# Optimization experiments

Hardware: AMD Instinct MI355X
Metric: run time of the kernel (lower is better)

## Reference

```python
import jax, jax.numpy as jnp
import numpy as np

B, N, IN_DIM, L_DIM, H_DIM, N_CLASSES, FLOW_LEN = 128, 512, 128, 64, 64, 10, 4


def setup_inputs() -> dict:
    key = jax.random.key(0)
    ks = jax.random.split(key, 20)
    s = 0.05
    return {
        "gs": jax.random.uniform(ks[0], (B, N, N), dtype=jnp.float32),
        "hs": jax.random.normal(ks[1], (B, N, IN_DIM), dtype=jnp.float32),
        "labels": jax.random.randint(ks[2], (B,), 0, N_CLASSES),
        "eps": jax.random.normal(ks[3], (B, N, 1), dtype=jnp.float32),
        "W_s": jax.random.normal(ks[4], (IN_DIM, L_DIM), dtype=jnp.float32) * s,
        "b_s": jnp.zeros((L_DIM,), jnp.float32),
        "W_mu": jax.random.normal(ks[5], (L_DIM, 1), dtype=jnp.float32) * s,
        "b_mu": jnp.zeros((1,), jnp.float32),
        "W_lv": jax.random.normal(ks[6], (L_DIM, 1), dtype=jnp.float32) * s,
        "b_lv": jnp.zeros((1,), jnp.float32),
        "W_dec": jax.random.normal(ks[7], (1, L_DIM), dtype=jnp.float32) * s,
        "b_dec": jnp.zeros((L_DIM,), jnp.float32),
        "W1": jax.random.normal(ks[8], (L_DIM, H_DIM), dtype=jnp.float32) * s,
        "b1": jnp.zeros((H_DIM,), jnp.float32),
        "W2": jax.random.normal(ks[9], (H_DIM, N_CLASSES), dtype=jnp.float32) * s,
        "b2": jnp.zeros((N_CLASSES,), jnp.float32),
        "beta": jax.random.uniform(ks[10], (1,), jnp.float32, 0.0, 100.0),
        "fw": jax.random.normal(ks[11], (FLOW_LEN,), dtype=jnp.float32) * 0.1,
        "fb": jax.random.normal(ks[12], (FLOW_LEN,), dtype=jnp.float32) * 0.1,
        "fs": jax.random.normal(ks[13], (FLOW_LEN,), dtype=jnp.float32) * 0.1,
    }


def reference(gs, hs, labels, eps, W_s, b_s, W_mu, b_mu, W_lv, b_lv,
              W_dec, b_dec, W1, b1, W2, b2, beta, fw, fb, fs):
    relu = jax.nn.relu
    # norm_g: g / g.sum(1) (torch broadcast divides column j by row-sum deg[j])
    deg = gs.sum(axis=2)                       # [B, N]
    g = gs / deg[:, None, :]                   # [B, N, N]

    def gcn(g, h, W, b):
        return relu(jnp.einsum('bij,bjf->bif', g, h) @ W + b)

    h = gcn(g, hs, W_s, b_s)                   # [B, N, L]
    r = h
    mu = gcn(g, h, W_mu, b_mu)                 # [B, N, 1]
    logvar = gcn(g, h, W_lv, b_lv)             # [B, N, 1]
    sigma = jnp.exp(0.5 * logvar)
    z0 = eps * sigma + mu                      # reparameterize (training)

    # 4-step planar flow on scalar latent; log-det accumulated on pre-transform z
    z = z0
    log_jac = jnp.zeros_like(z0)
    for k in range(FLOW_LEN):
        t = jnp.tanh(fw[k] * z + fb[k])
        det = 1.0 + fs[k] * fw[k] * (1.0 - t * t)
        log_jac = log_jac + jnp.log(jnp.abs(det) + 1e-7)
        z = z + fs[k] * t
    zk = z

    # KL = log q(z0) - log_jac - log p(zk), loggaussian = -0.5*((z-mu)/s)^2 - log(2.5 s)
    logq = -0.5 * ((z0 - mu) / sigma) ** 2 - jnp.log(2.5 * sigma)
    logp = -0.5 * zk ** 2 - jnp.log(jnp.float32(2.5))
    kl = logq - log_jac - logp                 # [B, N, 1]

    zs = jax.nn.sigmoid(beta * zk)             # [B, N, 1]
    d = gcn(g, zs, W_dec, b_dec)               # [B, N, L]
    hg = jnp.einsum('bnl,bn->bl', h, zs[..., 0])  # h.T @ zk, [B, L]

    # classify
    x = relu(hg @ W1 + b1)
    logits = jax.nn.log_softmax(x @ W2 + b2, axis=1)  # [B, C]

    nll = -jnp.mean(logits[jnp.arange(B), labels])
    mse = jnp.mean((r - d) ** 2)
    loss = nll + mse + kl.mean()
    preds = jnp.argmax(logits, axis=1)
    acc = jnp.mean((preds == labels).astype(jnp.float32))
    return jnp.stack([loss, acc])
```

## Files before the change

### kernel.cpp

```cpp
#include <hip/hip_runtime.h>
#include <hip/hip_bf16.h>

#define BB 128
#define NN 512
#define IND 128
#define LD 64
#define NC 10
#define FL 4
#define ROWS (BB*NN)

#define OFF_ACC 0
#define OFF_GSB 8
#define WS_NEED ((size_t)(OFF_GSB + (size_t)ROWS*256) * 4)

typedef __attribute__((ext_vector_type(8))) short short8v;
typedef __attribute__((ext_vector_type(4))) float f32x4;

__device__ inline float wave_reduce(float v) {
    #pragma unroll
    for (int m = 32; m; m >>= 1) v += __shfl_xor(v, m, 64);
    return v;
}

__device__ inline short f2bf(float f) {
    unsigned u = __float_as_uint(f);
    u += 0x7fff + ((u >> 16) & 1);
    return (short)(u >> 16);
}

__device__ inline float bf2f(short s) {
    return __uint_as_float(((unsigned)(unsigned short)s) << 16);
}

__global__ void k_zero(float* __restrict__ accums) {
    if (threadIdx.x < 8) accums[threadIdx.x] = 0.f;
}

template<bool BF>
__global__ __launch_bounds__(1024) void k_fused(
    const float* __restrict__ gs, const float* __restrict__ hs,
    const int* __restrict__ labels, const float* __restrict__ eps,
    const float* __restrict__ W_s, const float* __restrict__ b_s,
    const float* __restrict__ W_mu, const float* __restrict__ b_mu,
    const float* __restrict__ W_lv, const float* __restrict__ b_lv,
    const float* __restrict__ W_dec, const float* __restrict__ b_dec,
    const float* __restrict__ W1, const float* __restrict__ b1,
    const float* __restrict__ W2, const float* __restrict__ b2,
    const float* __restrict__ beta, const float* __restrict__ fw,
    const float* __restrict__ fb, const float* __restrict__ fs,
    unsigned short* __restrict__ gsb,
    float* __restrict__ accums, float* __restrict__ out)
{
    __shared__ unsigned short s_hwT[64 * 512];
    __shared__ unsigned short s_h[512 * 64];
    __shared__ float s_rdeg[NN];
    __shared__ float s_vm[NN], s_vv[NN];
    __shared__ float s_zs[NN], s_zss[NN];
    __shared__ float s_red[16 * 68];
    __shared__ float s_fin[48];

    const int tid = threadIdx.x, lane = tid & 63, wid = tid >> 6;
    const int b = blockIdx.x;

    for (int r = 0; r < 32; ++r) {
        int row = wid * 32 + r;
        const float4* gp = (const float4*)(gs + ((size_t)b * NN + row) * NN) + lane * 2;
        float4 a = gp[0], c = gp[1];
        float ssum = a.x + a.y + a.z + a.w + c.x + c.y + c.z + c.w;
        ssum = wave_reduce(ssum);
        if (lane == 0) s_rdeg[row] = 1.f / ssum;
        if constexpr (BF) {
            short8v v;
            v[0] = f2bf(a.x); v[1] = f2bf(a.y); v[2] = f2bf(a.z); v[3] = f2bf(a.w);
            v[4] = f2bf(c.x); v[5] = f2bf(c.y); v[6] = f2bf(c.z); v[7] = f2bf(c.w);
            *(short8v*)(gsb + ((size_t)b * NN + row) * NN + lane * 8) = v;
        }
    }

    unsigned short* sWT = s_h;
    {
        const float4* wp = (const float4*)W_s + tid * 2;
        float4 w0 = wp[0], w1 = wp[1];
        int k = tid >> 3, l0 = (tid & 7) * 8;
        float wv[8] = {w0.x, w0.y, w0.z, w0.w, w1.x, w1.y, w1.z, w1.w};
        #pragma unroll
        for (int e = 0; e < 8; ++e) {
            int l = l0 + e;
            int byte = (l * 256 + k * 2) ^ ((l & 7) << 4);
            *(unsigned short*)((char*)sWT + byte) = (unsigned short)f2bf(wv[e]);
        }
    }
    __syncthreads();

    {
        int n0 = wid * 32, cq = lane & 15, koq = lane >> 4;
        f32x4 accB[2][4] = {};
        #pragma unroll
        for (int kk = 0; kk < 4; ++kk) {
            short8v bf[4];
            #pragma unroll
            for (int lt = 0; lt < 4; ++lt) {
                int l = lt * 16 + cq;
                int byte = (l * 256 + (kk * 32 + koq * 8) * 2) ^ ((l & 7) << 4);
                bf[lt] = *(const short8v*)((char*)sWT + byte);
            }
            #pragma unroll
            for (int nt = 0; nt < 2; ++nt) {
                int row = n0 + nt * 16 + cq;
                const float4* hp = (const float4*)(hs + ((size_t)b * NN + row) * IND
                                                   + kk * 32 + koq * 8);
                float4 h0 = hp[0], h1 = hp[1];
                short8v a;
                a[0] = f2bf(h0.x); a[1] = f2bf(h0.y); a[2] = f2bf(h0.z); a[3] = f2bf(h0.w);
                a[4] = f2bf(h1.x); a[5] = f2bf(h1.y); a[6] = f2bf(h1.z); a[7] = f2bf(h1.w);
                #pragma unroll
                for (int lt = 0; lt < 4; ++lt)
                    accB[nt][lt] = __builtin_amdgcn_mfma_f32_16x16x32_bf16(a, bf[lt], accB[nt][lt], 0, 0, 0);
            }
        }
        int r0 = (lane >> 4) * 4;
        #pragma unroll
        for (int nt = 0; nt < 2; ++nt)
            #pragma unroll
            for (int lt = 0; lt < 4; ++lt)
                #pragma unroll
                for (int q = 0; q < 4; ++q) {
                    int n = n0 + nt * 16 + r0 + q;
                    int l = lt * 16 + cq;
                    int byte = (l * 1024 + n * 2) ^ ((l & 7) << 4);
                    *(unsigned short*)((char*)s_hwT + byte) =
                        (unsigned short)f2bf(accB[nt][lt][q] * s_rdeg[n]);
                }
    }
    __syncthreads();

    {
        int n0 = wid * 32, cq = lane & 15, koq = lane >> 4;
        f32x4 accC[2][4] = {};
        for (int kk = 0; kk < 16; ++kk) {
            short8v bf[4];
            #pragma unroll
            for (int lt = 0; lt < 4; ++lt) {
                int l = lt * 16 + cq;
                int byte = (l * 1024 + (kk * 32 + koq * 8) * 2) ^ ((l & 7) << 4);
                bf[lt] = *(const short8v*)((char*)s_hwT + byte);
            }
            #pragma unroll
            for (int nt = 0; nt < 2; ++nt) {
                int row = n0 + nt * 16 + cq;
                short8v a;
                if constexpr (BF) {
                    a = *(const short8v*)(gsb + ((size_t)b * NN + row) * NN + kk * 32 + koq * 8);
                } else {
                    const float4* gp = (const float4*)(gs + ((size_t)b * NN + row) * NN
                                                       + kk * 32 + koq * 8);
                    float4 g0 = gp[0], g1 = gp[1];
                    a[0] = f2bf(g0.x); a[1] = f2bf(g0.y); a[2] = f2bf(g0.z); a[3] = f2bf(g0.w);
                    a[4] = f2bf(g1.x); a[5] = f2bf(g1.y); a[6] = f2bf(g1.z); a[7] = f2bf(g1.w);
                }
                #pragma unroll
                for (int lt = 0; lt < 4; ++lt)
                    accC[nt][lt] = __builtin_amdgcn_mfma_f32_16x16x32_bf16(a, bf[lt], accC[nt][lt], 0, 0, 0);
            }
        }
        int r0 = (lane >> 4) * 4;
        float bsv[4];
        #pragma unroll
        for (int lt = 0; lt < 4; ++lt) bsv[lt] = b_s[lt * 16 + cq];
        #pragma unroll
        for (int nt = 0; nt < 2; ++nt)
            #pragma unroll
            for (int lt = 0; lt < 4; ++lt)
                #pragma unroll
                for (int q = 0; q < 4; ++q) {
                    int n = n0 + nt * 16 + r0 + q;
                    int l = lt * 16 + cq;
                    s_h[n * 64 + l] = (unsigned short)f2bf(fmaxf(accC[nt][lt][q] + bsv[lt], 0.f));
                }
    }
    __syncthreads();

    {
        int g16 = tid >> 4, l16 = tid & 15;
        float wmu[4], wlv[4];
        #pragma unroll
        for (int e = 0; e < 4; ++e) { wmu[e] = W_mu[l16 * 4 + e]; wlv[e] = W_lv[l16 * 4 + e]; }
        #pragma unroll
        for (int rr = 0; rr < 8; ++rr) {
            int row = g16 * 8 + rr;
            const unsigned short* hp = &s_h[row * 64 + l16 * 4];
            float pm = 0.f, pv = 0.f;
            #pragma unroll
            for (int e = 0; e < 4; ++e) {
                float hv = bf2f((short)hp[e]);
                pm += hv * wmu[e]; pv += hv * wlv[e];
            }
            #pragma unroll
            for (int m = 1; m <= 8; m <<= 1) {
                pm += __shfl_xor(pm, m, 64);
                pv += __shfl_xor(pv, m, 64);
            }
            if (l16 == 0) {
                float rd = s_rdeg[row];
                s_vm[row] = pm * rd;
                s_vv[row] = pv * rd;
            }
        }
    }
    __syncthreads();

    {
        float vmr[8], vvr[8];
        #pragma unroll
        for (int e = 0; e < 8; ++e) { vmr[e] = s_vm[lane * 8 + e]; vvr[e] = s_vv[lane * 8 + e]; }
        for (int r = 0; r < 32; ++r) {
            int row = wid * 32 + r;
            float sm, sv;
            if constexpr (BF) {
                short8v g8 = *(const short8v*)(gsb + ((size_t)b * NN + row) * NN + lane * 8);
                float g0 = bf2f(g8[0]), g1 = bf2f(g8[1]), g2 = bf2f(g8[2]), g3 = bf2f(g8[3]);
                float g4 = bf2f(g8[4]), g5 = bf2f(g8[5]), g6 = bf2f(g8[6]), g7 = bf2f(g8[7]);
                sm = g0*vmr[0]+g1*vmr[1]+g2*vmr[2]+g3*vmr[3]+g4*vmr[4]+g5*vmr[5]+g6*vmr[6]+g7*vmr[7];
                sv = g0*vvr[0]+g1*vvr[1]+g2*vvr[2]+g3*vvr[3]+g4*vvr[4]+g5*vvr[5]+g6*vvr[6]+g7*vvr[7];
            } else {
                const float4* gp = (const float4*)(gs + ((size_t)b * NN + row) * NN) + lane * 2;
                float4 ga = gp[0], gc = gp[1];
                sm = ga.x*vmr[0]+ga.y*vmr[1]+ga.z*vmr[2]+ga.w*vmr[3]
                   + gc.x*vmr[4]+gc.y*vmr[5]+gc.z*vmr[6]+gc.w*vmr[7];
                sv = ga.x*vvr[0]+ga.y*vvr[1]+ga.z*vvr[2]+ga.w*vvr[3]
                   + gc.x*vvr[4]+gc.y*vvr[5]+gc.z*vvr[6]+gc.w*vvr[7];
            }
            sm = wave_reduce(sm);
            sv = wave_reduce(sv);
            if (lane == 0) { s_zs[row] = sm; s_zss[row] = sv; }
        }
    }
    __syncthreads();

    float my_kl = 0.f;
    if (tid < NN) {
        float sm = s_zs[tid], sv = s_zss[tid];
        float mu = fmaxf(sm + b_mu[0], 0.f);
        float lv = fmaxf(sv + b_lv[0], 0.f);
        float sigma = expf(0.5f * lv);
        float z0 = eps[(size_t)b * NN + tid] * sigma + mu;
        float z = z0, lj = 0.f;
        #pragma unroll
        for (int k = 0; k < FL; ++k) {
            float tt = tanhf(fw[k] * z + fb[k]);
            float det = 1.f + fs[k] * fw[k] * (1.f - tt * tt);
            lj += logf(fabsf(det) + 1e-7f);
            z += fs[k] * tt;
        }
        float e0 = (z0 - mu) / sigma;
        float logq = -0.5f * e0 * e0 - logf(2.5f * sigma);
        float logp = -0.5f * z * z - logf(2.5f);
        my_kl = logq - lj - logp;
        float zv = 1.f / (1.f + expf(-beta[0] * z));
        s_zs[tid] = zv;
        s_zss[tid] = zv * s_rdeg[tid];
    }
    __syncthreads();

    float msacc = 0.f;
    {
        float wd = W_dec[lane], bd = b_dec[lane];
        float zr[8];
        #pragma unroll
        for (int e = 0; e < 8; ++e) zr[e] = s_zss[lane * 8 + e];
        for (int r = 0; r < 32; ++r) {
            int row = wid * 32 + r;
            float s;
            if constexpr (BF) {
                short8v g8 = *(const short8v*)(gsb + ((size_t)b * NN + row) * NN + lane * 8);
                s = bf2f(g8[0])*zr[0]+bf2f(g8[1])*zr[1]+bf2f(g8[2])*zr[2]+bf2f(g8[3])*zr[3]
                  + bf2f(g8[4])*zr[4]+bf2f(g8[5])*zr[5]+bf2f(g8[6])*zr[6]+bf2f(g8[7])*zr[7];
            } else {
                const float4* gp = (const float4*)(gs + ((size_t)b * NN + row) * NN) + lane * 2;
                float4 ga = gp[0], gc = gp[1];
                s = ga.x*zr[0]+ga.y*zr[1]+ga.z*zr[2]+ga.w*zr[3]
                  + gc.x*zr[4]+gc.y*zr[5]+gc.z*zr[6]+gc.w*zr[7];
            }
            s = wave_reduce(s);
            float dval = fmaxf(s * wd + bd, 0.f);
            float diff = bf2f((short)s_h[row * 64 + lane]) - dval;
            msacc += diff * diff;
        }
    }

    {
        float acc = 0.f;
        for (int r = 0; r < 32; ++r) {
            int row = wid * 32 + r;
            acc += bf2f((short)s_h[row * 64 + lane]) * s_zs[row];
        }
        s_red[wid * 68 + lane] = acc;
    }
    __syncthreads();

    {
        float kv = wave_reduce(my_kl);
        float mv = wave_reduce(msacc);
        if (lane == 0) { s_fin[wid] = kv; s_fin[16 + wid] = mv; }
    }
    if (wid == 0) {
        float hgv = 0.f;
        #pragma unroll
        for (int w = 0; w < 16; ++w) hgv += s_red[w * 68 + lane];
        s_red[lane] = hgv;
        float x = b1[lane];
        #pragma unroll 8
        for (int k = 0; k < LD; ++k) x += s_red[k] * W1[k * LD + lane];
        x = fmaxf(x, 0.f);
        s_red[256 + lane] = x;
        if (lane < NC) {
            float lg = b2[lane];
            #pragma unroll 8
            for (int k = 0; k < LD; ++k) lg += s_red[256 + k] * W2[k * NC + lane];
            s_fin[32 + lane] = lg;
        }
        if (lane == 0) {
            float mx = s_fin[32]; int pred = 0;
            #pragma unroll
            for (int c = 1; c < NC; ++c) if (s_fin[32 + c] > mx) { mx = s_fin[32 + c]; pred = c; }
            float se = 0.f;
            #pragma unroll
            for (int c = 0; c < NC; ++c) se += expf(s_fin[32 + c] - mx);
            int lab = labels[b];
            s_fin[44] = -(s_fin[32 + lab] - (mx + logf(se)));
            s_fin[45] = (pred == lab) ? 1.f : 0.f;
        }
    }
    __syncthreads();

    if (tid == 0) {
        float ksum = 0.f, msum = 0.f;
        #pragma unroll
        for (int w = 0; w < 16; ++w) { ksum += s_fin[w]; msum += s_fin[16 + w]; }
        atomicAdd(&accums[0], ksum);
        atomicAdd(&accums[1], msum);
        atomicAdd(&accums[2], s_fin[44]);
        atomicAdd(&accums[3], s_fin[45]);
        __threadfence();
        unsigned old = atomicAdd((unsigned*)&accums[4], 1u);
        if (old == BB - 1) {
            float kk = atomicAdd(&accums[0], 0.f);
            float mm = atomicAdd(&accums[1], 0.f);
            float nn = atomicAdd(&accums[2], 0.f);
            float aa = atomicAdd(&accums[3], 0.f);
            out[0] = nn / (float)BB
                   + mm / ((float)BB * NN * LD)
                   + kk / ((float)BB * NN);
            out[1] = aa / (float)BB;
        }
    }
}

extern "C" void kernel_launch(void* const* d_in, const int* in_sizes, int n_in,
                              void* d_out, int out_size, void* d_ws, size_t ws_size,
                              hipStream_t stream) {
    const float* gs    = (const float*)d_in[0];
    const float* hs    = (const float*)d_in[1];
    const int*   labels= (const int*)d_in[2];
    const float* eps   = (const float*)d_in[3];
    const float* W_s   = (const float*)d_in[4];
    const float* b_s   = (const float*)d_in[5];
    const float* W_mu  = (const float*)d_in[6];
    const float* b_mu  = (const float*)d_in[7];
    const float* W_lv  = (const float*)d_in[8];
    const float* b_lv  = (const float*)d_in[9];
    const float* W_dec = (const float*)d_in[10];
    const float* b_dec = (const float*)d_in[11];
    const float* W1    = (const float*)d_in[12];
    const float* b1    = (const float*)d_in[13];
    const float* W2    = (const float*)d_in[14];
    const float* b2    = (const float*)d_in[15];
    const float* beta  = (const float*)d_in[16];
    const float* fw    = (const float*)d_in[17];
    const float* fb    = (const float*)d_in[18];
    const float* fs    = (const float*)d_in[19];

    float* ws = (float*)d_ws;
    float* accums = ws + OFF_ACC;
    unsigned short* gsb = (unsigned short*)(ws + OFF_GSB);
    float* out = (float*)d_out;

    k_zero<<<1, 64, 0, stream>>>(accums);
    if (ws_size >= WS_NEED) {
        k_fused<true><<<BB, 1024, 0, stream>>>(gs, hs, labels, eps, W_s, b_s, W_mu, b_mu,
                                               W_lv, b_lv, W_dec, b_dec, W1, b1, W2, b2,
                                               beta, fw, fb, fs, gsb, accums, out);
    } else {
        k_fused<false><<<BB, 1024, 0, stream>>>(gs, hs, labels, eps, W_s, b_s, W_mu, b_mu,
                                                W_lv, b_lv, W_dec, b_dec, W1, b1, W2, b2,
                                                beta, fw, fb, fs, gsb, accums, out);
    }
}
```

Measured before the change: 116.8 us.

## Split fused per-batch kernel into multi-stage kernels with two blocks per graph

Replaces the single fused kernel (one 1024-thread block per graph) with a chain of kernels. A wide degree/bf16-conversion kernel is followed by GEMM, mu/flow, decoder and classifier kernels, each launching two blocks per graph that split the 512 rows. The aim is to fill more compute units than the 128 blocks did and to parallelise the degree pass across the whole device. In exchange, intermediates (h, vm/vv, zs, rdeg, partial hg) go through global workspace, there are extra launches, and each half-block recomputes the full h·W product.

```diff
diff --git a/kernel.cpp b/kernel.cpp
--- a/kernel.cpp
+++ b/kernel.cpp
@@ -8,9 +8,17 @@
 #define NC 10
 #define FL 4
 #define ROWS (BB*NN)
+#define HALF 256
 
 #define OFF_ACC 0
-#define OFF_GSB 8
+#define OFF_RDEG (OFF_ACC + 8)
+#define OFF_VM   (OFF_RDEG + ROWS)
+#define OFF_VV   (OFF_VM + ROWS)
+#define OFF_ZS   (OFF_VV + ROWS)
+#define OFF_ZSS  (OFF_ZS + ROWS)
+#define OFF_XHG  (OFF_ZSS + ROWS)
+#define OFF_H    (OFF_XHG + BB*128)
+#define OFF_GSB  (OFF_H + ROWS*32)
 #define WS_NEED ((size_t)(OFF_GSB + (size_t)ROWS*256) * 4)
 
 typedef __attribute__((ext_vector_type(8))) short short8v;
@@ -32,50 +40,43 @@
     return __uint_as_float(((unsigned)(unsigned short)s) << 16);
 }
 
-__global__ void k_zero(float* __restrict__ accums) {
-    if (threadIdx.x < 8) accums[threadIdx.x] = 0.f;
+__global__ __launch_bounds__(256) void k_deg(const float* __restrict__ gs,
+                                             float* __restrict__ rdeg,
+                                             float* __restrict__ accums,
+                                             unsigned short* __restrict__ gsb) {
+    if (blockIdx.x == 0 && threadIdx.x < 8) accums[threadIdx.x] = 0.f;
+    int t = threadIdx.x;
+    int row = blockIdx.x * 4 + (t >> 6), lane = t & 63;
+    const float4* r4 = (const float4*)(gs + (size_t)row * NN) + lane * 2;
+    float4 a = r4[0], b = r4[1];
+    float s = a.x + a.y + a.z + a.w + b.x + b.y + b.z + b.w;
+    float sr = wave_reduce(s);
+    if (lane == 0) rdeg[row] = 1.0f / sr;
+    if (gsb) {
+        short8v v;
+        v[0] = f2bf(a.x); v[1] = f2bf(a.y); v[2] = f2bf(a.z); v[3] = f2bf(a.w);
+        v[4] = f2bf(b.x); v[5] = f2bf(b.y); v[6] = f2bf(b.z); v[7] = f2bf(b.w);
+        *(short8v*)(gsb + (size_t)row * NN + lane * 8) = v;
+    }
 }
 
 template<bool BF>
-__global__ __launch_bounds__(1024) void k_fused(
-    const float* __restrict__ gs, const float* __restrict__ hs,
-    const int* __restrict__ labels, const float* __restrict__ eps,
-    const float* __restrict__ W_s, const float* __restrict__ b_s,
-    const float* __restrict__ W_mu, const float* __restrict__ b_mu,
-    const float* __restrict__ W_lv, const float* __restrict__ b_lv,
-    const float* __restrict__ W_dec, const float* __restrict__ b_dec,
-    const float* __restrict__ W1, const float* __restrict__ b1,
-    const float* __restrict__ W2, const float* __restrict__ b2,
-    const float* __restrict__ beta, const float* __restrict__ fw,
-    const float* __restrict__ fb, const float* __restrict__ fs,
-    unsigned short* __restrict__ gsb,
-    float* __restrict__ accums, float* __restrict__ out)
+__global__ __launch_bounds__(1024) void k_hwgemm(
+    const float* __restrict__ gs, const unsigned short* __restrict__ gsb,
+    const float* __restrict__ hs, const float* __restrict__ W_s,
+    const float* __restrict__ b_s, const float* __restrict__ W_mu,
+    const float* __restrict__ W_lv, const float* __restrict__ rdeg_ws,
+    unsigned short* __restrict__ h_ws, float* __restrict__ vm_ws,
+    float* __restrict__ vv_ws)
 {
     __shared__ unsigned short s_hwT[64 * 512];
-    __shared__ unsigned short s_h[512 * 64];
+    __shared__ unsigned short s_h[HALF * 64];
     __shared__ float s_rdeg[NN];
-    __shared__ float s_vm[NN], s_vv[NN];
-    __shared__ float s_zs[NN], s_zss[NN];
-    __shared__ float s_red[16 * 68];
-    __shared__ float s_fin[48];
 
     const int tid = threadIdx.x, lane = tid & 63, wid = tid >> 6;
-    const int b = blockIdx.x;
-
-    for (int r = 0; r < 32; ++r) {
-        int row = wid * 32 + r;
-        const float4* gp = (const float4*)(gs + ((size_t)b * NN + row) * NN) + lane * 2;
-        float4 a = gp[0], c = gp[1];
-        float ssum = a.x + a.y + a.z + a.w + c.x + c.y + c.z + c.w;
-        ssum = wave_reduce(ssum);
-        if (lane == 0) s_rdeg[row] = 1.f / ssum;
-        if constexpr (BF) {
-            short8v v;
-            v[0] = f2bf(a.x); v[1] = f2bf(a.y); v[2] = f2bf(a.z); v[3] = f2bf(a.w);
-            v[4] = f2bf(c.x); v[5] = f2bf(c.y); v[6] = f2bf(c.z); v[7] = f2bf(c.w);
-            *(short8v*)(gsb + ((size_t)b * NN + row) * NN + lane * 8) = v;
-        }
-    }
+    const int b = blockIdx.x >> 1, p = blockIdx.x & 1, rbase = p * HALF;
+
+    if (tid < NN) s_rdeg[tid] = rdeg_ws[(size_t)b * NN + tid];
 
     unsigned short* sWT = s_h;
     {
@@ -118,6 +119,7 @@
                     accB[nt][lt] = __builtin_amdgcn_mfma_f32_16x16x32_bf16(a, bf[lt], accB[nt][lt], 0, 0, 0);
             }
         }
+        __syncthreads();
         int r0 = (lane >> 4) * 4;
         #pragma unroll
         for (int nt = 0; nt < 2; ++nt)
@@ -135,8 +137,11 @@
     __syncthreads();
 
     {
-        int n0 = wid * 32, cq = lane & 15, koq = lane >> 4;
-        f32x4 accC[2][4] = {};
+        int cq = lane & 15, koq = lane >> 4;
+        int rowl = wid * 16 + cq, rowg = rbase + rowl;
+        const unsigned short* A16 = gsb + ((size_t)b * NN + rowg) * NN + koq * 8;
+        const float* A32 = gs + ((size_t)b * NN + rowg) * NN + koq * 8;
+        f32x4 accC[4] = {};
         for (int kk = 0; kk < 16; ++kk) {
             short8v bf[4];
             #pragma unroll
@@ -145,40 +150,41 @@
                 int byte = (l * 1024 + (kk * 32 + koq * 8) * 2) ^ ((l & 7) << 4);
                 bf[lt] = *(const short8v*)((char*)s_hwT + byte);
             }
-            #pragma unroll
-            for (int nt = 0; nt < 2; ++nt) {
-                int row = n0 + nt * 16 + cq;
-                short8v a;
-                if constexpr (BF) {
-                    a = *(const short8v*)(gsb + ((size_t)b * NN + row) * NN + kk * 32 + koq * 8);
-                } else {
-                    const float4* gp = (const float4*)(gs + ((size_t)b * NN + row) * NN
-                                                       + kk * 32 + koq * 8);
-                    float4 g0 = gp[0], g1 = gp[1];
-                    a[0] = f2bf(g0.x); a[1] = f2bf(g0.y); a[2] = f2bf(g0.z); a[3] = f2bf(g0.w);
-                    a[4] = f2bf(g1.x); a[5] = f2bf(g1.y); a[6] = f2bf(g1.z); a[7] = f2bf(g1.w);
-                }
-                #pragma unroll
-                for (int lt = 0; lt < 4; ++lt)
-                    accC[nt][lt] = __builtin_amdgcn_mfma_f32_16x16x32_bf16(a, bf[lt], accC[nt][lt], 0, 0, 0);
-            }
+            short8v a;
+            if constexpr (BF) {
+                a = *(const short8v*)(A16 + kk * 32);
+            } else {
+                const float4* gp = (const float4*)(A32 + kk * 32);
+                float4 g0 = gp[0], g1 = gp[1];
+                a[0] = f2bf(g0.x); a[1] = f2bf(g0.y); a[2] = f2bf(g0.z); a[3] = f2bf(g0.w);
+                a[4] = f2bf(g1.x); a[5] = f2bf(g1.y); a[6] = f2bf(g1.z); a[7] = f2bf(g1.w);
+            }
+            #pragma unroll
+            for (int lt = 0; lt < 4; ++lt)
+                accC[lt] = __builtin_amdgcn_mfma_f32_16x16x32_bf16(a, bf[lt], accC[lt], 0, 0, 0);
         }
         int r0 = (lane >> 4) * 4;
         float bsv[4];
         #pragma unroll
         for (int lt = 0; lt < 4; ++lt) bsv[lt] = b_s[lt * 16 + cq];
         #pragma unroll
-        for (int nt = 0; nt < 2; ++nt)
-            #pragma unroll
-            for (int lt = 0; lt < 4; ++lt)
-                #pragma unroll
-                for (int q = 0; q < 4; ++q) {
-                    int n = n0 + nt * 16 + r0 + q;
-                    int l = lt * 16 + cq;
-                    s_h[n * 64 + l] = (unsigned short)f2bf(fmaxf(accC[nt][lt][q] + bsv[lt], 0.f));
-                }
-    }
-    __syncthreads();
+        for (int lt = 0; lt < 4; ++lt)
+            #pragma unroll
+            for (int q = 0; q < 4; ++q) {
+                int nloc = wid * 16 + r0 + q;
+                int l = lt * 16 + cq;
+                s_h[nloc * 64 + l] = (unsigned short)f2bf(fmaxf(accC[lt][q] + bsv[lt], 0.f));
+            }
+    }
+    __syncthreads();
+
+    {
+        int rowl = tid >> 2, off = (tid & 3) * 16;
+        unsigned short* dst = h_ws + ((size_t)(b * NN + rbase + rowl)) * 64 + off;
+        const unsigned short* src = &s_h[rowl * 64 + off];
+        *(short8v*)dst = *(const short8v*)src;
+        *(short8v*)(dst + 8) = *(const short8v*)(src + 8);
+    }
 
     {
         int g16 = tid >> 4, l16 = tid & 15;
@@ -186,9 +192,9 @@
         #pragma unroll
         for (int e = 0; e < 4; ++e) { wmu[e] = W_mu[l16 * 4 + e]; wlv[e] = W_lv[l16 * 4 + e]; }
         #pragma unroll
-        for (int rr = 0; rr < 8; ++rr) {
-            int row = g16 * 8 + rr;
-            const unsigned short* hp = &s_h[row * 64 + l16 * 4];
+        for (int rr = 0; rr < 4; ++rr) {
+            int rowl = g16 * 4 + rr;
+            const unsigned short* hp = &s_h[rowl * 64 + l16 * 4];
             float pm = 0.f, pv = 0.f;
             #pragma unroll
             for (int e = 0; e < 4; ++e) {
@@ -201,49 +207,66 @@
                 pv += __shfl_xor(pv, m, 64);
             }
             if (l16 == 0) {
-                float rd = s_rdeg[row];
-                s_vm[row] = pm * rd;
-                s_vv[row] = pv * rd;
-            }
-        }
-    }
-    __syncthreads();
-
-    {
-        float vmr[8], vvr[8];
-        #pragma unroll
-        for (int e = 0; e < 8; ++e) { vmr[e] = s_vm[lane * 8 + e]; vvr[e] = s_vv[lane * 8 + e]; }
-        for (int r = 0; r < 32; ++r) {
-            int row = wid * 32 + r;
-            float sm, sv;
-            if constexpr (BF) {
-                short8v g8 = *(const short8v*)(gsb + ((size_t)b * NN + row) * NN + lane * 8);
-                float g0 = bf2f(g8[0]), g1 = bf2f(g8[1]), g2 = bf2f(g8[2]), g3 = bf2f(g8[3]);
-                float g4 = bf2f(g8[4]), g5 = bf2f(g8[5]), g6 = bf2f(g8[6]), g7 = bf2f(g8[7]);
-                sm = g0*vmr[0]+g1*vmr[1]+g2*vmr[2]+g3*vmr[3]+g4*vmr[4]+g5*vmr[5]+g6*vmr[6]+g7*vmr[7];
-                sv = g0*vvr[0]+g1*vvr[1]+g2*vvr[2]+g3*vvr[3]+g4*vvr[4]+g5*vvr[5]+g6*vvr[6]+g7*vvr[7];
-            } else {
-                const float4* gp = (const float4*)(gs + ((size_t)b * NN + row) * NN) + lane * 2;
-                float4 ga = gp[0], gc = gp[1];
-                sm = ga.x*vmr[0]+ga.y*vmr[1]+ga.z*vmr[2]+ga.w*vmr[3]
-                   + gc.x*vmr[4]+gc.y*vmr[5]+gc.z*vmr[6]+gc.w*vmr[7];
-                sv = ga.x*vvr[0]+ga.y*vvr[1]+ga.z*vvr[2]+ga.w*vvr[3]
-                   + gc.x*vvr[4]+gc.y*vvr[5]+gc.z*vvr[6]+gc.w*vvr[7];
-            }
-            sm = wave_reduce(sm);
-            sv = wave_reduce(sv);
-            if (lane == 0) { s_zs[row] = sm; s_zss[row] = sv; }
-        }
+                float rd = s_rdeg[rbase + rowl];
+                vm_ws[(size_t)b * NN + rbase + rowl] = pm * rd;
+                vv_ws[(size_t)b * NN + rbase + rowl] = pv * rd;
+            }
+        }
+    }
+}
+
+template<bool BF>
+__global__ __launch_bounds__(1024) void k_muflow(
+    const float* __restrict__ gs, const unsigned short* __restrict__ gsb,
+    const float* __restrict__ vm_ws, const float* __restrict__ vv_ws,
+    const float* __restrict__ eps, const float* __restrict__ b_mu,
+    const float* __restrict__ b_lv, const float* __restrict__ beta,
+    const float* __restrict__ fw, const float* __restrict__ fb,
+    const float* __restrict__ fs, const float* __restrict__ rdeg_ws,
+    float* __restrict__ zs_ws, float* __restrict__ zss_ws,
+    float* __restrict__ accums)
+{
+    __shared__ float s_mp[HALF], s_lp[HALF];
+    __shared__ float s_fin[16];
+    const int tid = threadIdx.x, lane = tid & 63, wid = tid >> 6;
+    const int b = blockIdx.x >> 1, p = blockIdx.x & 1, rbase = p * HALF;
+
+    float vmr[8], vvr[8];
+    #pragma unroll
+    for (int e = 0; e < 8; ++e) {
+        vmr[e] = vm_ws[(size_t)b * NN + lane * 8 + e];
+        vvr[e] = vv_ws[(size_t)b * NN + lane * 8 + e];
+    }
+    for (int r = 0; r < 16; ++r) {
+        int rowl = wid * 16 + r, rowg = rbase + rowl;
+        float sm, sv;
+        if constexpr (BF) {
+            short8v g8 = *(const short8v*)(gsb + ((size_t)b * NN + rowg) * NN + lane * 8);
+            float g0 = bf2f(g8[0]), g1 = bf2f(g8[1]), g2 = bf2f(g8[2]), g3 = bf2f(g8[3]);
+            float g4 = bf2f(g8[4]), g5 = bf2f(g8[5]), g6 = bf2f(g8[6]), g7 = bf2f(g8[7]);
+            sm = g0*vmr[0]+g1*vmr[1]+g2*vmr[2]+g3*vmr[3]+g4*vmr[4]+g5*vmr[5]+g6*vmr[6]+g7*vmr[7];
+            sv = g0*vvr[0]+g1*vvr[1]+g2*vvr[2]+g3*vvr[3]+g4*vvr[4]+g5*vvr[5]+g6*vvr[6]+g7*vvr[7];
+        } else {
+            const float4* gp = (const float4*)(gs + ((size_t)b * NN + rowg) * NN) + lane * 2;
+            float4 ga = gp[0], gc = gp[1];
+            sm = ga.x*vmr[0]+ga.y*vmr[1]+ga.z*vmr[2]+ga.w*vmr[3]
+               + gc.x*vmr[4]+gc.y*vmr[5]+gc.z*vmr[6]+gc.w*vmr[7];
+            sv = ga.x*vvr[0]+ga.y*vvr[1]+ga.z*vvr[2]+ga.w*vvr[3]
+               + gc.x*vvr[4]+gc.y*vvr[5]+gc.z*vvr[6]+gc.w*vvr[7];
+        }
+        sm = wave_reduce(sm);
+        sv = wave_reduce(sv);
+        if (lane == 0) { s_mp[rowl] = sm; s_lp[rowl] = sv; }
     }
     __syncthreads();
 
     float my_kl = 0.f;
-    if (tid < NN) {
-        float sm = s_zs[tid], sv = s_zss[tid];
-        float mu = fmaxf(sm + b_mu[0], 0.f);
-        float lv = fmaxf(sv + b_lv[0], 0.f);
+    if (tid < HALF) {
+        int rowg = rbase + tid;
+        float mu = fmaxf(s_mp[tid] + b_mu[0], 0.f);
+        float lv = fmaxf(s_lp[tid] + b_lv[0], 0.f);
         float sigma = expf(0.5f * lv);
-        float z0 = eps[(size_t)b * NN + tid] * sigma + mu;
+        float z0 = eps[(size_t)b * NN + rowg] * sigma + mu;
         float z = z0, lj = 0.f;
         #pragma unroll
         for (int k = 0; k < FL; ++k) {
@@ -257,90 +280,116 @@
         float logp = -0.5f * z * z - logf(2.5f);
         my_kl = logq - lj - logp;
         float zv = 1.f / (1.f + expf(-beta[0] * z));
-        s_zs[tid] = zv;
-        s_zss[tid] = zv * s_rdeg[tid];
-    }
-    __syncthreads();
-
-    float msacc = 0.f;
-    {
-        float wd = W_dec[lane], bd = b_dec[lane];
-        float zr[8];
-        #pragma unroll
-        for (int e = 0; e < 8; ++e) zr[e] = s_zss[lane * 8 + e];
-        for (int r = 0; r < 32; ++r) {
-            int row = wid * 32 + r;
-            float s;
-            if constexpr (BF) {
-                short8v g8 = *(const short8v*)(gsb + ((size_t)b * NN + row) * NN + lane * 8);
-                s = bf2f(g8[0])*zr[0]+bf2f(g8[1])*zr[1]+bf2f(g8[2])*zr[2]+bf2f(g8[3])*zr[3]
-                  + bf2f(g8[4])*zr[4]+bf2f(g8[5])*zr[5]+bf2f(g8[6])*zr[6]+bf2f(g8[7])*zr[7];
-            } else {
-                const float4* gp = (const float4*)(gs + ((size_t)b * NN + row) * NN) + lane * 2;
-                float4 ga = gp[0], gc = gp[1];
-                s = ga.x*zr[0]+ga.y*zr[1]+ga.z*zr[2]+ga.w*zr[3]
-                  + gc.x*zr[4]+gc.y*zr[5]+gc.z*zr[6]+gc.w*zr[7];
-            }
-            s = wave_reduce(s);
-            float dval = fmaxf(s * wd + bd, 0.f);
-            float diff = bf2f((short)s_h[row * 64 + lane]) - dval;
-            msacc += diff * diff;
-        }
-    }
-
-    {
-        float acc = 0.f;
-        for (int r = 0; r < 32; ++r) {
-            int row = wid * 32 + r;
-            acc += bf2f((short)s_h[row * 64 + lane]) * s_zs[row];
-        }
-        s_red[wid * 68 + lane] = acc;
-    }
-    __syncthreads();
-
-    {
-        float kv = wave_reduce(my_kl);
-        float mv = wave_reduce(msacc);
-        if (lane == 0) { s_fin[wid] = kv; s_fin[16 + wid] = mv; }
+        float rd = rdeg_ws[(size_t)b * NN + rowg];
+        zs_ws[(size_t)b * NN + rowg] = zv;
+        zss_ws[(size_t)b * NN + rowg] = zv * rd;
+    }
+    float kv = wave_reduce(my_kl);
+    if (lane == 0) s_fin[wid] = kv;
+    __syncthreads();
+    if (tid == 0) {
+        float ks = 0.f;
+        #pragma unroll
+        for (int w = 0; w < 16; ++w) ks += s_fin[w];
+        atomicAdd(&accums[0], ks);
+    }
+}
+
+template<bool BF>
+__global__ __launch_bounds__(1024) void k_dec(
+    const float* __restrict__ gs, const unsigned short* __restrict__ gsb,
+    const float* __restrict__ zss_ws, const float* __restrict__ zs_ws,
+    const unsigned short* __restrict__ h_ws, const float* __restrict__ W_dec,
+    const float* __restrict__ b_dec, float* __restrict__ accums,
+    float* __restrict__ xhg)
+{
+    __shared__ float s_zs[HALF];
+    __shared__ float s_red[16 * 68];
+    __shared__ float s_fin[16];
+    const int tid = threadIdx.x, lane = tid & 63, wid = tid >> 6;
+    const int b = blockIdx.x >> 1, p = blockIdx.x & 1, rbase = p * HALF;
+
+    if (tid < HALF) s_zs[tid] = zs_ws[(size_t)b * NN + rbase + tid];
+    float zr[8];
+    #pragma unroll
+    for (int e = 0; e < 8; ++e) zr[e] = zss_ws[(size_t)b * NN + lane * 8 + e];
+    float wd = W_dec[lane], bd = b_dec[lane];
+    __syncthreads();
+
+    float msacc = 0.f, hgacc = 0.f;
+    for (int r = 0; r < 16; ++r) {
+        int rowl = wid * 16 + r, rowg = rbase + rowl;
+        float s;
+        if constexpr (BF) {
+            short8v g8 = *(const short8v*)(gsb + ((size_t)b * NN + rowg) * NN + lane * 8);
+            s = bf2f(g8[0])*zr[0]+bf2f(g8[1])*zr[1]+bf2f(g8[2])*zr[2]+bf2f(g8[3])*zr[3]
+              + bf2f(g8[4])*zr[4]+bf2f(g8[5])*zr[5]+bf2f(g8[6])*zr[6]+bf2f(g8[7])*zr[7];
+        } else {
+            const float4* gp = (const float4*)(gs + ((size_t)b * NN + rowg) * NN) + lane * 2;
+            float4 ga = gp[0], gc = gp[1];
+            s = ga.x*zr[0]+ga.y*zr[1]+ga.z*zr[2]+ga.w*zr[3]
+              + gc.x*zr[4]+gc.y*zr[5]+gc.z*zr[6]+gc.w*zr[7];
+        }
+        s = wave_reduce(s);
+        float dval = fmaxf(s * wd + bd, 0.f);
+        float hval = bf2f((short)h_ws[((size_t)b * NN + rowg) * 64 + lane]);
+        float diff = hval - dval;
+        msacc += diff * diff;
+        hgacc += hval * s_zs[rowl];
+    }
+    s_red[wid * 68 + lane] = hgacc;
+    float mv = wave_reduce(msacc);
+    if (lane == 0) s_fin[wid] = mv;
+    __syncthreads();
+    if (tid == 0) {
+        float ms = 0.f;
+        #pragma unroll
+        for (int w = 0; w < 16; ++w) ms += s_fin[w];
+        atomicAdd(&accums[1], ms);
     }
     if (wid == 0) {
         float hgv = 0.f;
         #pragma unroll
         for (int w = 0; w < 16; ++w) hgv += s_red[w * 68 + lane];
-        s_red[lane] = hgv;
-        float x = b1[lane];
+        xhg[(size_t)b * 128 + p * 64 + lane] = hgv;
+    }
+}
+
+__global__ __launch_bounds__(64) void k_cls(const float* __restrict__ xhg,
+                                            const float* __restrict__ W1,
+                                            const float* __restrict__ b1,
+                                            const float* __restrict__ W2,
+                                            const float* __restrict__ b2,
+                                            const int* __restrict__ labels,
+                                            float* __restrict__ accums,
+                                            float* __restrict__ out)
+{
+    __shared__ float s_hg[64], s_x[64], s_lg[12];
+    int b = blockIdx.x, l = threadIdx.x;
+    s_hg[l] = xhg[(size_t)b * 128 + l] + xhg[(size_t)b * 128 + 64 + l];
+    __syncthreads();
+    float x = b1[l];
+    #pragma unroll 8
+    for (int k = 0; k < LD; ++k) x += s_hg[k] * W1[k * LD + l];
+    s_x[l] = fmaxf(x, 0.f);
+    __syncthreads();
+    if (l < NC) {
+        float lg = b2[l];
         #pragma unroll 8
-        for (int k = 0; k < LD; ++k) x += s_red[k] * W1[k * LD + lane];
-        x = fmaxf(x, 0.f);
-        s_red[256 + lane] = x;
-        if (lane < NC) {
-            float lg = b2[lane];
-            #pragma unroll 8
-            for (int k = 0; k < LD; ++k) lg += s_red[256 + k] * W2[k * NC + lane];
-            s_fin[32 + lane] = lg;
-        }
-        if (lane == 0) {
-            float mx = s_fin[32]; int pred = 0;
-            #pragma unroll
-            for (int c = 1; c < NC; ++c) if (s_fin[32 + c] > mx) { mx = s_fin[32 + c]; pred = c; }
-            float se = 0.f;
-            #pragma unroll
-            for (int c = 0; c < NC; ++c) se += expf(s_fin[32 + c] - mx);
-            int lab = labels[b];
-            s_fin[44] = -(s_fin[32 + lab] - (mx + logf(se)));
-            s_fin[45] = (pred == lab) ? 1.f : 0.f;
-        }
-    }
-    __syncthreads();
-
-    if (tid == 0) {
-        float ksum = 0.f, msum = 0.f;
-        #pragma unroll
-        for (int w = 0; w < 16; ++w) { ksum += s_fin[w]; msum += s_fin[16 + w]; }
-        atomicAdd(&accums[0], ksum);
-        atomicAdd(&accums[1], msum);
-        atomicAdd(&accums[2], s_fin[44]);
-        atomicAdd(&accums[3], s_fin[45]);
+        for (int k = 0; k < LD; ++k) lg += s_x[k] * W2[k * NC + l];
+        s_lg[l] = lg;
+    }
+    __syncthreads();
+    if (l == 0) {
+        float mx = s_lg[0]; int pred = 0;
+        #pragma unroll
+        for (int c = 1; c < NC; ++c) if (s_lg[c] > mx) { mx = s_lg[c]; pred = c; }
+        float se = 0.f;
+        #pragma unroll
+        for (int c = 0; c < NC; ++c) se += expf(s_lg[c] - mx);
+        int lab = labels[b];
+        atomicAdd(&accums[2], -(s_lg[lab] - (mx + logf(se))));
+        if (pred == lab) atomicAdd(&accums[3], 1.0f);
         __threadfence();
         unsigned old = atomicAdd((unsigned*)&accums[4], 1u);
         if (old == BB - 1) {
@@ -380,19 +429,37 @@
     const float* fb    = (const float*)d_in[18];
     const float* fs    = (const float*)d_in[19];
 
-    float* ws = (float*)d_ws;
-    float* accums = ws + OFF_ACC;
-    unsigned short* gsb = (unsigned short*)(ws + OFF_GSB);
+    float* ws      = (float*)d_ws;
+    float* accums  = ws + OFF_ACC;
+    float* rdeg    = ws + OFF_RDEG;
+    float* vm_ws   = ws + OFF_VM;
+    float* vv_ws   = ws + OFF_VV;
+    float* zs_ws   = ws + OFF_ZS;
+    float* zss_ws  = ws + OFF_ZSS;
+    float* xhg     = ws + OFF_XHG;
+    unsigned short* h_ws = (unsigned short*)(ws + OFF_H);
+    unsigned short* gsb  = (unsigned short*)(ws + OFF_GSB);
     float* out = (float*)d_out;
 
-    k_zero<<<1, 64, 0, stream>>>(accums);
-    if (ws_size >= WS_NEED) {
-        k_fused<true><<<BB, 1024, 0, stream>>>(gs, hs, labels, eps, W_s, b_s, W_mu, b_mu,
-                                               W_lv, b_lv, W_dec, b_dec, W1, b1, W2, b2,
-                                               beta, fw, fb, fs, gsb, accums, out);
+    bool big = ws_size >= WS_NEED;
+
+    k_deg<<<ROWS / 4, 256, 0, stream>>>(gs, rdeg, accums, big ? gsb : nullptr);
+    if (big) {
+        k_hwgemm<true><<<2 * BB, 1024, 0, stream>>>(gs, gsb, hs, W_s, b_s, W_mu, W_lv,
+                                                    rdeg, h_ws, vm_ws, vv_ws);
+        k_muflow<true><<<2 * BB, 1024, 0, stream>>>(gs, gsb, vm_ws, vv_ws, eps, b_mu, b_lv,
+                                                    beta, fw, fb, fs, rdeg, zs_ws, zss_ws,
+                                                    accums);
+        k_dec<true><<<2 * BB, 1024, 0, stream>>>(gs, gsb, zss_ws, zs_ws, h_ws, W_dec, b_dec,
+                                                 accums, xhg);
     } else {
-        k_fused<false><<<BB, 1024, 0, stream>>>(gs, hs, labels, eps, W_s, b_s, W_mu, b_mu,
-                                                W_lv, b_lv, W_dec, b_dec, W1, b1, W2, b2,
-                                                beta, fw, fb, fs, gsb, accums, out);
-    }
-}
+        k_hwgemm<false><<<2 * BB, 1024, 0, stream>>>(gs, gsb, hs, W_s, b_s, W_mu, W_lv,
+                                                     rdeg, h_ws, vm_ws, vv_ws);
+        k_muflow<false><<<2 * BB, 1024, 0, stream>>>(gs, gsb, vm_ws, vv_ws, eps, b_mu, b_lv,
+                                                     beta, fw, fb, fs, rdeg, zs_ws, zss_ws,
+                                                     accums);
+        k_dec<false><<<2 * BB, 1024, 0, stream>>>(gs, gsb, zss_ws, zs_ws, h_ws, W_dec, b_dec,
+                                                  accums, xhg);
+    }
+    k_cls<<<BB, 64, 0, stream>>>(xhg, W1, b1, W2, b2, labels, accums, out);
+}
```

Result: faster. 103.6 us (-11.3%).
